# Performance work log

Hardware: AMD Instinct MI355X
Metric: run time of the kernel (lower is better)

Reference implementation:

```python
import jax, jax.numpy as jnp
import numpy as np

N_NODES = 100000
N_EDGES = 1600000
N_GRAPHS = 4096
IN_DIM = 14
HID = 128


def setup_inputs() -> dict:
    key = jax.random.key(0)
    ks = jax.random.split(key, 12)
    x = jax.random.normal(ks[0], (N_NODES, IN_DIM), dtype=jnp.float32)
    edge_index = jax.random.randint(ks[1], (2, N_EDGES), 0, N_NODES, dtype=jnp.int64)
    batch = jnp.sort(jax.random.randint(ks[2], (N_NODES,), 0, N_GRAPHS, dtype=jnp.int64))

    def lin(k, fan_in, fan_out):
        bound = 1.0 / np.sqrt(fan_in)
        kw, kb = jax.random.split(k)
        W = jax.random.uniform(kw, (fan_in, fan_out), minval=-bound, maxval=bound, dtype=jnp.float32)
        b = jax.random.uniform(kb, (fan_out,), minval=-bound, maxval=bound, dtype=jnp.float32)
        return W, b

    W1a, b1a = lin(ks[3], IN_DIM, HID)
    W1b, b1b = lin(ks[4], HID, HID)
    W2a, b2a = lin(ks[5], HID, HID)
    W2b, b2b = lin(ks[6], HID, HID)
    Wout, bout = lin(ks[7], HID, HID)
    return dict(x=x, edge_index=edge_index, batch=batch,
                W1a=W1a, b1a=b1a, W1b=W1b, b1b=b1b,
                W2a=W2a, b2a=b2a, W2b=W2b, b2b=b2b,
                Wout=Wout, bout=bout)


def _gin_conv(x, src, dst, Wa, ba, Wb, bb):
    # aggregate: sum of neighbor features x[src] scattered to dst; eps = 0
    agg = jax.ops.segment_sum(x[src], dst, num_segments=N_NODES)
    h = x + agg  # (1 + eps) * x + sum_j x_j, eps=0
    h = jax.nn.relu(h @ Wa + ba)
    return h @ Wb + bb


def reference(x, edge_index, batch, W1a, b1a, W1b, b1b, W2a, b2a, W2b, b2b, Wout, bout):
    src, dst = edge_index[0], edge_index[1]
    h = jax.nn.relu(_gin_conv(x, src, dst, W1a, b1a, W1b, b1b))
    h = jax.nn.relu(_gin_conv(h, src, dst, W2a, b2a, W2b, b2b))
    # global mean pool over graphs
    sums = jax.ops.segment_sum(h, batch, num_segments=N_GRAPHS)          # [G, HID]
    cnts = jax.ops.segment_sum(jnp.ones((h.shape[0],), h.dtype), batch, num_segments=N_GRAPHS)
    pooled = sums / jnp.maximum(cnts, 1.0)[:, None]
    # dropout is identity in eval mode
    return pooled @ Wout + bout
```

## Files before the change

kernel.cpp:

```cpp
#include <hip/hip_runtime.h>
#include <hip/hip_bf16.h>

#define NODES  100000
#define EDGES  1600000
#define GRAPHS 4096
#define HID    128
#define INDIM  14
#define NPART  8
#define PART_SZ ((NODES + NPART - 1) / NPART)
#define BPG    256
#define CSTRIDE 64
#define LDST   136

typedef float f32x4 __attribute__((ext_vector_type(4)));
typedef short bf16x8 __attribute__((ext_vector_type(8)));
typedef int   i32x4 __attribute__((ext_vector_type(4)));

__device__ __forceinline__ unsigned packbf(float a, float b) {
    __hip_bfloat162 t;
    t.x = __float2bfloat16(a);
    t.y = __float2bfloat16(b);
    return *(unsigned*)&t;
}
__device__ __forceinline__ void acc8(float* a, uint4 v) {
    a[0] += __uint_as_float(v.x << 16);
    a[1] += __uint_as_float(v.x & 0xffff0000u);
    a[2] += __uint_as_float(v.y << 16);
    a[3] += __uint_as_float(v.y & 0xffff0000u);
    a[4] += __uint_as_float(v.z << 16);
    a[5] += __uint_as_float(v.z & 0xffff0000u);
    a[6] += __uint_as_float(v.w << 16);
    a[7] += __uint_as_float(v.w & 0xffff0000u);
}


__global__ void k_zero_int(int* __restrict__ p, int n) {
    int i = blockIdx.x * 256 + threadIdx.x;
    if (i < n) p[i] = 0;
}

__global__ __launch_bounds__(256) void k_fill_fx(const i32x4* __restrict__ src4,
                                                 const i32x4* __restrict__ dst4,
                                                 int* __restrict__ cnt,
                                                 int* __restrict__ csr) {
    const int g = blockIdx.x & (NPART - 1);
    const int blk = blockIdx.x >> 3;
    const int lo = g * PART_SZ;
    const int n4 = EDGES / 4;
    for (int e4 = blk * 256 + threadIdx.x; e4 < n4; e4 += BPG * 256) {
        i32x4 d = __builtin_nontemporal_load(&dst4[e4]);
        i32x4 s = __builtin_nontemporal_load(&src4[e4]);
#pragma unroll
        for (int j = 0; j < 4; j++) {
            int dj = d[j];
            if ((unsigned)(dj - lo) < PART_SZ) {
                int pos = atomicAdd(&cnt[dj], 1);
                if (pos < CSTRIDE) csr[dj * CSTRIDE + pos] = s[j];
            }
        }
    }
}


__global__ void k_w_cvt4(const float* __restrict__ Wa, const float* __restrict__ Wb,
                         const float* __restrict__ Wc, const float* __restrict__ Wd,
                         __hip_bfloat16* __restrict__ Ta, __hip_bfloat16* __restrict__ Tb,
                         __hip_bfloat16* __restrict__ Tc, __hip_bfloat16* __restrict__ Td) {
    int which = blockIdx.x >> 6;
    int idx = (blockIdx.x & 63) * 256 + threadIdx.x;
    const float* W = which == 0 ? Wa : which == 1 ? Wb : which == 2 ? Wc : Wd;
    __hip_bfloat16* T = which == 0 ? Ta : which == 1 ? Tb : which == 2 ? Tc : Td;
    int n = idx & 127, k = idx >> 7;
    T[n * HID + k] = __float2bfloat16(W[k * HID + n]);
}

template <int RELU, int TO_LDS>
__device__ __forceinline__ void mfma_slice16(const __hip_bfloat16* lds_in,
                                             const __hip_bfloat16* __restrict__ Wt,
                                             const float* __restrict__ bias,
                                             __hip_bfloat16* lds_out,
                                             __hip_bfloat16* __restrict__ gout,
                                             int row0, int tid) {
    const int wave = tid >> 6;
    const int lane = tid & 63;
    const int rl = lane & 15;
    const int kb = lane >> 4;

    bf16x8 afrag[4];
#pragma unroll
    for (int kc = 0; kc < 4; kc++)
        afrag[kc] = *(const bf16x8*)(lds_in + rl * LDST + kc * 32 + kb * 8);

#pragma unroll
    for (int s = 0; s < 2; s++) {
        const int n = wave * 2 + s;
        f32x4 acc = (f32x4){0.f, 0.f, 0.f, 0.f};
        const __hip_bfloat16* Bp = Wt + (size_t)(n * 16 + rl) * HID + kb * 8;
#pragma unroll
        for (int kc = 0; kc < 4; kc++) {
            bf16x8 bfrag = *(const bf16x8*)(Bp + kc * 32);
            acc = __builtin_amdgcn_mfma_f32_16x16x32_bf16(afrag[kc], bfrag, acc, 0, 0, 0);
        }
        const int col = n * 16 + rl;
        const float bv = bias[col];
#pragma unroll
        for (int j = 0; j < 4; j++) {
            int rloc = kb * 4 + j;
            float v = acc[j] + bv;
            if (RELU) v = fmaxf(v, 0.f);
            if (TO_LDS)
                lds_out[rloc * LDST + col] = __float2bfloat16(v);
            else
                gout[(size_t)(row0 + rloc) * HID + col] = __float2bfloat16(v);
        }
    }
}


__global__ __launch_bounds__(256) void k_l1(const float* __restrict__ x,
                                            const int* __restrict__ cnt,
                                            const int* __restrict__ csr,
                                            const float* __restrict__ W1a,
                                            const float* __restrict__ b1a,
                                            const __hip_bfloat16* __restrict__ Wt1b,
                                            const float* __restrict__ b1b,
                                            __hip_bfloat16* __restrict__ h1) {
    __shared__ float p14[16][16];
    __shared__ __hip_bfloat16 t[16 * LDST];
    const int row0 = blockIdx.x * 16;
    const int tid = threadIdx.x;

    {
        int n = tid >> 4, d = tid & 15;
        int node = row0 + n;
        if (d < INDIM) {
            int len = cnt[node];
            if (len > CSTRIDE) len = CSTRIDE;
            const int* cp = csr + (size_t)node * CSTRIDE;
            float acc = x[node * INDIM + d];
            int e = 0;
            for (; e + 7 < len; e += 8) {
                int s0 = cp[e], s1 = cp[e + 1], s2 = cp[e + 2], s3 = cp[e + 3];
                int s4 = cp[e + 4], s5 = cp[e + 5], s6 = cp[e + 6], s7 = cp[e + 7];
                float v0 = x[s0 * INDIM + d], v1 = x[s1 * INDIM + d];
                float v2 = x[s2 * INDIM + d], v3 = x[s3 * INDIM + d];
                float v4 = x[s4 * INDIM + d], v5 = x[s5 * INDIM + d];
                float v6 = x[s6 * INDIM + d], v7 = x[s7 * INDIM + d];
                acc += ((v0 + v1) + (v2 + v3)) + ((v4 + v5) + (v6 + v7));
            }
            for (; e + 3 < len; e += 4) {
                int s0 = cp[e], s1 = cp[e + 1], s2 = cp[e + 2], s3 = cp[e + 3];
                acc += x[s0 * INDIM + d] + x[s1 * INDIM + d] +
                       x[s2 * INDIM + d] + x[s3 * INDIM + d];
            }
            for (; e < len; e++) acc += x[cp[e] * INDIM + d];
            p14[n][d] = acc;
        }
    }
    __syncthreads();

    for (int i = tid; i < 512; i += 256) {
        int r = i >> 5, c4 = (i & 31) << 2;
        float4 bv = *(const float4*)&b1a[c4];
        float ax = bv.x, ay = bv.y, az = bv.z, aw = bv.w;
#pragma unroll
        for (int k = 0; k < INDIM; k++) {
            float a = p14[r][k];
            float4 w = *(const float4*)&W1a[k * HID + c4];
            ax += a * w.x; ay += a * w.y; az += a * w.z; aw += a * w.w;
        }
        unsigned p0 = packbf(fmaxf(ax, 0.f), fmaxf(ay, 0.f));
        unsigned p1 = packbf(fmaxf(az, 0.f), fmaxf(aw, 0.f));
        *(uint2*)&t[r * LDST + c4] = make_uint2(p0, p1);
    }
    __syncthreads();

    mfma_slice16<1, 0>(t, Wt1b, b1b, nullptr, h1, row0, tid);
}


__global__ __launch_bounds__(256) void k_l2(const uint4* __restrict__ H,
                                            const int* __restrict__ cnt,
                                            const int* __restrict__ csr,
                                            const __hip_bfloat16* __restrict__ Wt2a,
                                            const float* __restrict__ b2a,
                                            const __hip_bfloat16* __restrict__ Wt2b,
                                            const float* __restrict__ b2b,
                                            __hip_bfloat16* __restrict__ h2) {
    __shared__ __hip_bfloat16 ta[16 * LDST];
    __shared__ __hip_bfloat16 tb[16 * LDST];
    const int row0 = blockIdx.x * 16;
    const int tid = threadIdx.x;

    {
        int n = tid >> 4, q = tid & 15;
        int node = row0 + n;
        int len = cnt[node];
        if (len > CSTRIDE) len = CSTRIDE;
        const int* cp = csr + (size_t)node * CSTRIDE;
        float a[8];
        uint4 v = H[(size_t)node * 16 + q];
        a[0] = __uint_as_float(v.x << 16);
        a[1] = __uint_as_float(v.x & 0xffff0000u);
        a[2] = __uint_as_float(v.y << 16);
        a[3] = __uint_as_float(v.y & 0xffff0000u);
        a[4] = __uint_as_float(v.z << 16);
        a[5] = __uint_as_float(v.z & 0xffff0000u);
        a[6] = __uint_as_float(v.w << 16);
        a[7] = __uint_as_float(v.w & 0xffff0000u);
        int e = 0;
        for (; e + 7 < len; e += 8) {
            uint4 v0 = H[(size_t)cp[e + 0] * 16 + q];
            uint4 v1 = H[(size_t)cp[e + 1] * 16 + q];
            uint4 v2 = H[(size_t)cp[e + 2] * 16 + q];
            uint4 v3 = H[(size_t)cp[e + 3] * 16 + q];
            uint4 v4 = H[(size_t)cp[e + 4] * 16 + q];
            uint4 v5 = H[(size_t)cp[e + 5] * 16 + q];
            uint4 v6 = H[(size_t)cp[e + 6] * 16 + q];
            uint4 v7 = H[(size_t)cp[e + 7] * 16 + q];
            acc8(a, v0); acc8(a, v1); acc8(a, v2); acc8(a, v3);
            acc8(a, v4); acc8(a, v5); acc8(a, v6); acc8(a, v7);
        }
        for (; e + 3 < len; e += 4) {
            uint4 v0 = H[(size_t)cp[e + 0] * 16 + q];
            uint4 v1 = H[(size_t)cp[e + 1] * 16 + q];
            uint4 v2 = H[(size_t)cp[e + 2] * 16 + q];
            uint4 v3 = H[(size_t)cp[e + 3] * 16 + q];
            acc8(a, v0); acc8(a, v1); acc8(a, v2); acc8(a, v3);
        }
        for (; e < len; e++) {
            uint4 vv = H[(size_t)cp[e] * 16 + q];
            acc8(a, vv);
        }
        uint4 o;
        o.x = packbf(a[0], a[1]);
        o.y = packbf(a[2], a[3]);
        o.z = packbf(a[4], a[5]);
        o.w = packbf(a[6], a[7]);
        *(uint4*)&ta[n * LDST + q * 8] = o;
    }
    __syncthreads();

    mfma_slice16<1, 1>(ta, Wt2a, b2a, tb, nullptr, row0, tid);
    __syncthreads();

    mfma_slice16<1, 0>(tb, Wt2b, b2b, nullptr, h2, row0, tid);
}


__global__ __launch_bounds__(256) void k_head(const __hip_bfloat16* __restrict__ A,
                                              const __hip_bfloat16* __restrict__ Wt,
                                              const float* __restrict__ bias,
                                              float* __restrict__ out) {
    const int wave = threadIdx.x >> 6;
    const int lane = threadIdx.x & 63;
    const int row0 = blockIdx.x * 64 + wave * 16;
    const int rl = lane & 15;
    const int kb = lane >> 4;

    const __hip_bfloat16* Ap = A + (size_t)(row0 + rl) * HID + kb * 8;
    bf16x8 afrag[4];
#pragma unroll
    for (int kc = 0; kc < 4; kc++) afrag[kc] = *(const bf16x8*)(Ap + kc * 32);

#pragma unroll
    for (int n = 0; n < 8; n++) {
        f32x4 acc = (f32x4){0.f, 0.f, 0.f, 0.f};
        const __hip_bfloat16* Bp = Wt + (size_t)(n * 16 + rl) * HID + kb * 8;
#pragma unroll
        for (int kc = 0; kc < 4; kc++) {
            bf16x8 bfrag = *(const bf16x8*)(Bp + kc * 32);
            acc = __builtin_amdgcn_mfma_f32_16x16x32_bf16(afrag[kc], bfrag, acc, 0, 0, 0);
        }
        const int col = n * 16 + rl;
        const float bv = bias[col];
#pragma unroll
        for (int j = 0; j < 4; j++)
            out[(size_t)(row0 + kb * 4 + j) * HID + col] = acc[j] + bv;
    }
}


__device__ __forceinline__ int lower_bound_i(const int* __restrict__ a, int n, int key) {
    int lo = 0, hi = n;
    while (lo < hi) {
        int mid = (lo + hi) >> 1;
        if (a[mid] < key) lo = mid + 1; else hi = mid;
    }
    return lo;
}

__global__ __launch_bounds__(128) void k_pool(const __hip_bfloat16* __restrict__ H,
                                              const int* __restrict__ batch,
                                              __hip_bfloat16* __restrict__ pooled) {
    int g = blockIdx.x;
    int d = threadIdx.x;
    int lo = lower_bound_i(batch, NODES, g);
    int hi = lower_bound_i(batch, NODES, g + 1);
    float acc = 0.f;
    for (int i = lo; i < hi; i++) acc += __bfloat162float(H[(size_t)i * HID + d]);
    float cnt = (float)(hi - lo);
    pooled[(size_t)g * HID + d] = __float2bfloat16(acc / fmaxf(cnt, 1.0f));
}


extern "C" void kernel_launch(void* const* d_in, const int* in_sizes, int n_in,
                              void* d_out, int out_size, void* d_ws, size_t ws_size,
                              hipStream_t stream) {
    const float* x     = (const float*)d_in[0];
    const int*   ei    = (const int*)d_in[1];
    const int*   batch = (const int*)d_in[2];
    const float* W1a = (const float*)d_in[3];
    const float* b1a = (const float*)d_in[4];
    const float* W1b = (const float*)d_in[5];
    const float* b1b = (const float*)d_in[6];
    const float* W2a = (const float*)d_in[7];
    const float* b2a = (const float*)d_in[8];
    const float* W2b = (const float*)d_in[9];
    const float* b2b = (const float*)d_in[10];
    const float* Wout = (const float*)d_in[11];
    const float* bout = (const float*)d_in[12];

    const int* src = ei;
    const int* dst = ei + EDGES;

    char* w = (char*)d_ws;
    auto alloc = [&](size_t bytes) {
        void* p = (void*)w;
        w += (bytes + 255) & ~(size_t)255;
        return p;
    };
    __hip_bfloat16* h1 = (__hip_bfloat16*)alloc((size_t)NODES * HID * 2);
    __hip_bfloat16* h2 = (__hip_bfloat16*)alloc((size_t)NODES * HID * 2);
    __hip_bfloat16* pooled = (__hip_bfloat16*)alloc((size_t)GRAPHS * HID * 2);
    __hip_bfloat16* Wt1b = (__hip_bfloat16*)alloc(HID * HID * 2);
    __hip_bfloat16* Wt2a = (__hip_bfloat16*)alloc(HID * HID * 2);
    __hip_bfloat16* Wt2b = (__hip_bfloat16*)alloc(HID * HID * 2);
    __hip_bfloat16* Wtout = (__hip_bfloat16*)alloc(HID * HID * 2);
    int* cnt = (int*)alloc((size_t)NODES * 4);
    int* csr = (int*)alloc((size_t)NODES * CSTRIDE * 4);
    float* out = (float*)d_out;

    k_w_cvt4<<<256, 256, 0, stream>>>(W1b, W2a, W2b, Wout, Wt1b, Wt2a, Wt2b, Wtout);

    k_zero_int<<<(NODES + 255) / 256, 256, 0, stream>>>(cnt, NODES);
    k_fill_fx<<<NPART * BPG, 256, 0, stream>>>((const i32x4*)src, (const i32x4*)dst, cnt, csr);

    k_l1<<<NODES / 16, 256, 0, stream>>>(x, cnt, csr, W1a, b1a, Wt1b, b1b, h1);
    k_l2<<<NODES / 16, 256, 0, stream>>>((const uint4*)h1, cnt, csr, Wt2a, b2a, Wt2b, b2b, h2);

    k_pool<<<GRAPHS, 128, 0, stream>>>(h2, batch, pooled);
    k_head<<<GRAPHS / 64, 256, 0, stream>>>(pooled, Wtout, bout, out);
}
```

Baseline: 274.1 us.

## Slice hidden features into 16-column planes for cache-local layer-2 gather

Layer 1 now writes h1 in a sliced layout of eight planes of 16 bf16 columns each. A new gather kernel aggregates neighbours one slice at a time, so each slice's working set (about 3.2MB) can stay cache-resident during the random gathers. The aggregation is split from the two layer-2 GEMMs, which move to a separate MFMA kernel over 64-row tiles. The input x is also pre-converted to padded bf16, and the weight-conversion and counter-zeroing launches are merged into one prep kernel. In exchange the aggregate is written to and read back from global memory, one extra launch is added, and x is rounded to bf16 before aggregation.

```diff
diff --git a/kernel.cpp b/kernel.cpp
--- a/kernel.cpp
+++ b/kernel.cpp
@@ -11,6 +11,7 @@
 #define BPG    256
 #define CSTRIDE 64
 #define LDST   136
+#define NSLICE 8
 
 typedef float f32x4 __attribute__((ext_vector_type(4)));
 typedef short bf16x8 __attribute__((ext_vector_type(8)));
@@ -22,22 +23,38 @@
     t.y = __float2bfloat16(b);
     return *(unsigned*)&t;
 }
-__device__ __forceinline__ void acc8(float* a, uint4 v) {
-    a[0] += __uint_as_float(v.x << 16);
-    a[1] += __uint_as_float(v.x & 0xffff0000u);
-    a[2] += __uint_as_float(v.y << 16);
-    a[3] += __uint_as_float(v.y & 0xffff0000u);
-    a[4] += __uint_as_float(v.z << 16);
-    a[5] += __uint_as_float(v.z & 0xffff0000u);
-    a[6] += __uint_as_float(v.w << 16);
-    a[7] += __uint_as_float(v.w & 0xffff0000u);
-}
-
-
-__global__ void k_zero_int(int* __restrict__ p, int n) {
-    int i = blockIdx.x * 256 + threadIdx.x;
-    if (i < n) p[i] = 0;
-}
+__device__ __forceinline__ float2 upk(unsigned u) {
+    float2 f;
+    f.x = __uint_as_float(u << 16);
+    f.y = __uint_as_float(u & 0xffff0000u);
+    return f;
+}
+
+
+__global__ void k_prep(const float* __restrict__ W1b, const float* __restrict__ W2a,
+                       const float* __restrict__ W2b, const float* __restrict__ Wout,
+                       __hip_bfloat16* __restrict__ T1b, __hip_bfloat16* __restrict__ T2a,
+                       __hip_bfloat16* __restrict__ T2b, __hip_bfloat16* __restrict__ Tout,
+                       const float* __restrict__ x, __hip_bfloat16* __restrict__ xb,
+                       int* __restrict__ cnt) {
+    int b = blockIdx.x;
+    if (b < 256) {
+        int which = b >> 6;
+        int idx = (b & 63) * 256 + threadIdx.x;
+        const float* W = which == 0 ? W1b : which == 1 ? W2a : which == 2 ? W2b : Wout;
+        __hip_bfloat16* T = which == 0 ? T1b : which == 1 ? T2a : which == 2 ? T2b : Tout;
+        int n = idx & 127, k = idx >> 7;
+        T[n * HID + k] = __float2bfloat16(W[k * HID + n]);
+    } else if (b < 256 + 6250) {
+        int idx = (b - 256) * 256 + threadIdx.x;
+        int node = idx >> 4, c = idx & 15;
+        xb[idx] = __float2bfloat16(c < INDIM ? x[node * INDIM + c] : 0.f);
+    } else {
+        int i = (b - 6506) * 256 + threadIdx.x;
+        if (i < NODES) cnt[i] = 0;
+    }
+}
+
 
 __global__ __launch_bounds__(256) void k_fill_fx(const i32x4* __restrict__ src4,
                                                  const i32x4* __restrict__ dst4,
@@ -62,69 +79,14 @@
 }
 
 
-__global__ void k_w_cvt4(const float* __restrict__ Wa, const float* __restrict__ Wb,
-                         const float* __restrict__ Wc, const float* __restrict__ Wd,
-                         __hip_bfloat16* __restrict__ Ta, __hip_bfloat16* __restrict__ Tb,
-                         __hip_bfloat16* __restrict__ Tc, __hip_bfloat16* __restrict__ Td) {
-    int which = blockIdx.x >> 6;
-    int idx = (blockIdx.x & 63) * 256 + threadIdx.x;
-    const float* W = which == 0 ? Wa : which == 1 ? Wb : which == 2 ? Wc : Wd;
-    __hip_bfloat16* T = which == 0 ? Ta : which == 1 ? Tb : which == 2 ? Tc : Td;
-    int n = idx & 127, k = idx >> 7;
-    T[n * HID + k] = __float2bfloat16(W[k * HID + n]);
-}
-
-template <int RELU, int TO_LDS>
-__device__ __forceinline__ void mfma_slice16(const __hip_bfloat16* lds_in,
-                                             const __hip_bfloat16* __restrict__ Wt,
-                                             const float* __restrict__ bias,
-                                             __hip_bfloat16* lds_out,
-                                             __hip_bfloat16* __restrict__ gout,
-                                             int row0, int tid) {
-    const int wave = tid >> 6;
-    const int lane = tid & 63;
-    const int rl = lane & 15;
-    const int kb = lane >> 4;
-
-    bf16x8 afrag[4];
-#pragma unroll
-    for (int kc = 0; kc < 4; kc++)
-        afrag[kc] = *(const bf16x8*)(lds_in + rl * LDST + kc * 32 + kb * 8);
-
-#pragma unroll
-    for (int s = 0; s < 2; s++) {
-        const int n = wave * 2 + s;
-        f32x4 acc = (f32x4){0.f, 0.f, 0.f, 0.f};
-        const __hip_bfloat16* Bp = Wt + (size_t)(n * 16 + rl) * HID + kb * 8;
-#pragma unroll
-        for (int kc = 0; kc < 4; kc++) {
-            bf16x8 bfrag = *(const bf16x8*)(Bp + kc * 32);
-            acc = __builtin_amdgcn_mfma_f32_16x16x32_bf16(afrag[kc], bfrag, acc, 0, 0, 0);
-        }
-        const int col = n * 16 + rl;
-        const float bv = bias[col];
-#pragma unroll
-        for (int j = 0; j < 4; j++) {
-            int rloc = kb * 4 + j;
-            float v = acc[j] + bv;
-            if (RELU) v = fmaxf(v, 0.f);
-            if (TO_LDS)
-                lds_out[rloc * LDST + col] = __float2bfloat16(v);
-            else
-                gout[(size_t)(row0 + rloc) * HID + col] = __float2bfloat16(v);
-        }
-    }
-}
-
-
-__global__ __launch_bounds__(256) void k_l1(const float* __restrict__ x,
+__global__ __launch_bounds__(256) void k_l1(const __hip_bfloat16* __restrict__ xb,
                                             const int* __restrict__ cnt,
                                             const int* __restrict__ csr,
                                             const float* __restrict__ W1a,
                                             const float* __restrict__ b1a,
                                             const __hip_bfloat16* __restrict__ Wt1b,
                                             const float* __restrict__ b1b,
-                                            __hip_bfloat16* __restrict__ h1) {
+                                            __hip_bfloat16* __restrict__ h1b) {
     __shared__ float p14[16][16];
     __shared__ __hip_bfloat16 t[16 * LDST];
     const int row0 = blockIdx.x * 16;
@@ -137,23 +99,17 @@
             int len = cnt[node];
             if (len > CSTRIDE) len = CSTRIDE;
             const int* cp = csr + (size_t)node * CSTRIDE;
-            float acc = x[node * INDIM + d];
+            float acc = __bfloat162float(xb[node * 16 + d]);
             int e = 0;
-            for (; e + 7 < len; e += 8) {
-                int s0 = cp[e], s1 = cp[e + 1], s2 = cp[e + 2], s3 = cp[e + 3];
-                int s4 = cp[e + 4], s5 = cp[e + 5], s6 = cp[e + 6], s7 = cp[e + 7];
-                float v0 = x[s0 * INDIM + d], v1 = x[s1 * INDIM + d];
-                float v2 = x[s2 * INDIM + d], v3 = x[s3 * INDIM + d];
-                float v4 = x[s4 * INDIM + d], v5 = x[s5 * INDIM + d];
-                float v6 = x[s6 * INDIM + d], v7 = x[s7 * INDIM + d];
-                acc += ((v0 + v1) + (v2 + v3)) + ((v4 + v5) + (v6 + v7));
-            }
             for (; e + 3 < len; e += 4) {
                 int s0 = cp[e], s1 = cp[e + 1], s2 = cp[e + 2], s3 = cp[e + 3];
-                acc += x[s0 * INDIM + d] + x[s1 * INDIM + d] +
-                       x[s2 * INDIM + d] + x[s3 * INDIM + d];
+                float v0 = __bfloat162float(xb[s0 * 16 + d]);
+                float v1 = __bfloat162float(xb[s1 * 16 + d]);
+                float v2 = __bfloat162float(xb[s2 * 16 + d]);
+                float v3 = __bfloat162float(xb[s3 * 16 + d]);
+                acc += (v0 + v1) + (v2 + v3);
             }
-            for (; e < len; e++) acc += x[cp[e] * INDIM + d];
+            for (; e < len; e++) acc += __bfloat162float(xb[cp[e] * 16 + d]);
             p14[n][d] = acc;
         }
     }
@@ -175,108 +131,144 @@
     }
     __syncthreads();
 
-    mfma_slice16<1, 0>(t, Wt1b, b1b, nullptr, h1, row0, tid);
-}
-
-
-__global__ __launch_bounds__(256) void k_l2(const uint4* __restrict__ H,
-                                            const int* __restrict__ cnt,
-                                            const int* __restrict__ csr,
+    {
+        const int wave = tid >> 6;
+        const int lane = tid & 63;
+        const int rl = lane & 15;
+        const int kb = lane >> 4;
+        bf16x8 afrag[4];
+#pragma unroll
+        for (int kc = 0; kc < 4; kc++)
+            afrag[kc] = *(const bf16x8*)(t + rl * LDST + kc * 32 + kb * 8);
+#pragma unroll
+        for (int s = 0; s < 2; s++) {
+            const int n = wave * 2 + s;
+            f32x4 acc = (f32x4){0.f, 0.f, 0.f, 0.f};
+            const __hip_bfloat16* Bp = Wt1b + (size_t)(n * 16 + rl) * HID + kb * 8;
+#pragma unroll
+            for (int kc = 0; kc < 4; kc++) {
+                bf16x8 bfrag = *(const bf16x8*)(Bp + kc * 32);
+                acc = __builtin_amdgcn_mfma_f32_16x16x32_bf16(afrag[kc], bfrag, acc, 0, 0, 0);
+            }
+            const float bv = b1b[n * 16 + rl];
+#pragma unroll
+            for (int j = 0; j < 4; j++) {
+                int node = row0 + kb * 4 + j;
+                float v = fmaxf(acc[j] + bv, 0.f);
+                h1b[((size_t)n * NODES + node) * 16 + rl] = __float2bfloat16(v);
+            }
+        }
+    }
+}
+
+
+__global__ __launch_bounds__(256) void k_g(const unsigned* __restrict__ Hb,
+                                           const int* __restrict__ cnt,
+                                           const int* __restrict__ csr,
+                                           unsigned* __restrict__ Ab) {
+    const int s = blockIdx.x & 7;
+    const int tile = blockIdx.x >> 3;
+    const int nl = threadIdx.x >> 3;
+    const int q = threadIdx.x & 7;
+    const int node = tile * 32 + nl;
+    const unsigned* base = Hb + (size_t)s * NODES * 8;
+    int len = cnt[node];
+    if (len > CSTRIDE) len = CSTRIDE;
+    const int* cp = csr + (size_t)node * CSTRIDE;
+    float2 acc = upk(base[(size_t)node * 8 + q]);
+    int e = 0;
+    for (; e + 7 < len; e += 8) {
+        unsigned v0 = base[(size_t)cp[e + 0] * 8 + q];
+        unsigned v1 = base[(size_t)cp[e + 1] * 8 + q];
+        unsigned v2 = base[(size_t)cp[e + 2] * 8 + q];
+        unsigned v3 = base[(size_t)cp[e + 3] * 8 + q];
+        unsigned v4 = base[(size_t)cp[e + 4] * 8 + q];
+        unsigned v5 = base[(size_t)cp[e + 5] * 8 + q];
+        unsigned v6 = base[(size_t)cp[e + 6] * 8 + q];
+        unsigned v7 = base[(size_t)cp[e + 7] * 8 + q];
+        float2 f0 = upk(v0), f1 = upk(v1), f2 = upk(v2), f3 = upk(v3);
+        float2 f4 = upk(v4), f5 = upk(v5), f6 = upk(v6), f7 = upk(v7);
+        acc.x += ((f0.x + f1.x) + (f2.x + f3.x)) + ((f4.x + f5.x) + (f6.x + f7.x));
+        acc.y += ((f0.y + f1.y) + (f2.y + f3.y)) + ((f4.y + f5.y) + (f6.y + f7.y));
+    }
+    for (; e + 3 < len; e += 4) {
+        unsigned v0 = base[(size_t)cp[e + 0] * 8 + q];
+        unsigned v1 = base[(size_t)cp[e + 1] * 8 + q];
+        unsigned v2 = base[(size_t)cp[e + 2] * 8 + q];
+        unsigned v3 = base[(size_t)cp[e + 3] * 8 + q];
+        float2 f0 = upk(v0), f1 = upk(v1), f2 = upk(v2), f3 = upk(v3);
+        acc.x += (f0.x + f1.x) + (f2.x + f3.x);
+        acc.y += (f0.y + f1.y) + (f2.y + f3.y);
+    }
+    for (; e < len; e++) {
+        float2 f = upk(base[(size_t)cp[e] * 8 + q]);
+        acc.x += f.x;
+        acc.y += f.y;
+    }
+    Ab[(size_t)s * NODES * 8 + (size_t)node * 8 + q] = packbf(acc.x, acc.y);
+}
+
+
+__global__ __launch_bounds__(256) void k_g2(const __hip_bfloat16* __restrict__ aggb,
                                             const __hip_bfloat16* __restrict__ Wt2a,
                                             const float* __restrict__ b2a,
                                             const __hip_bfloat16* __restrict__ Wt2b,
                                             const float* __restrict__ b2b,
                                             __hip_bfloat16* __restrict__ h2) {
-    __shared__ __hip_bfloat16 ta[16 * LDST];
-    __shared__ __hip_bfloat16 tb[16 * LDST];
-    const int row0 = blockIdx.x * 16;
-    const int tid = threadIdx.x;
-
-    {
-        int n = tid >> 4, q = tid & 15;
-        int node = row0 + n;
-        int len = cnt[node];
-        if (len > CSTRIDE) len = CSTRIDE;
-        const int* cp = csr + (size_t)node * CSTRIDE;
-        float a[8];
-        uint4 v = H[(size_t)node * 16 + q];
-        a[0] = __uint_as_float(v.x << 16);
-        a[1] = __uint_as_float(v.x & 0xffff0000u);
-        a[2] = __uint_as_float(v.y << 16);
-        a[3] = __uint_as_float(v.y & 0xffff0000u);
-        a[4] = __uint_as_float(v.z << 16);
-        a[5] = __uint_as_float(v.z & 0xffff0000u);
-        a[6] = __uint_as_float(v.w << 16);
-        a[7] = __uint_as_float(v.w & 0xffff0000u);
-        int e = 0;
-        for (; e + 7 < len; e += 8) {
-            uint4 v0 = H[(size_t)cp[e + 0] * 16 + q];
-            uint4 v1 = H[(size_t)cp[e + 1] * 16 + q];
-            uint4 v2 = H[(size_t)cp[e + 2] * 16 + q];
-            uint4 v3 = H[(size_t)cp[e + 3] * 16 + q];
-            uint4 v4 = H[(size_t)cp[e + 4] * 16 + q];
-            uint4 v5 = H[(size_t)cp[e + 5] * 16 + q];
-            uint4 v6 = H[(size_t)cp[e + 6] * 16 + q];
-            uint4 v7 = H[(size_t)cp[e + 7] * 16 + q];
-            acc8(a, v0); acc8(a, v1); acc8(a, v2); acc8(a, v3);
-            acc8(a, v4); acc8(a, v5); acc8(a, v6); acc8(a, v7);
-        }
-        for (; e + 3 < len; e += 4) {
-            uint4 v0 = H[(size_t)cp[e + 0] * 16 + q];
-            uint4 v1 = H[(size_t)cp[e + 1] * 16 + q];
-            uint4 v2 = H[(size_t)cp[e + 2] * 16 + q];
-            uint4 v3 = H[(size_t)cp[e + 3] * 16 + q];
-            acc8(a, v0); acc8(a, v1); acc8(a, v2); acc8(a, v3);
-        }
-        for (; e < len; e++) {
-            uint4 vv = H[(size_t)cp[e] * 16 + q];
-            acc8(a, vv);
-        }
-        uint4 o;
-        o.x = packbf(a[0], a[1]);
-        o.y = packbf(a[2], a[3]);
-        o.z = packbf(a[4], a[5]);
-        o.w = packbf(a[6], a[7]);
-        *(uint4*)&ta[n * LDST + q * 8] = o;
-    }
-    __syncthreads();
-
-    mfma_slice16<1, 1>(ta, Wt2a, b2a, tb, nullptr, row0, tid);
-    __syncthreads();
-
-    mfma_slice16<1, 0>(tb, Wt2b, b2b, nullptr, h2, row0, tid);
-}
-
-
-__global__ __launch_bounds__(256) void k_head(const __hip_bfloat16* __restrict__ A,
-                                              const __hip_bfloat16* __restrict__ Wt,
-                                              const float* __restrict__ bias,
-                                              float* __restrict__ out) {
+    __shared__ __hip_bfloat16 t[64 * LDST];
     const int wave = threadIdx.x >> 6;
     const int lane = threadIdx.x & 63;
-    const int row0 = blockIdx.x * 64 + wave * 16;
     const int rl = lane & 15;
     const int kb = lane >> 4;
-
-    const __hip_bfloat16* Ap = A + (size_t)(row0 + rl) * HID + kb * 8;
+    const int row0 = blockIdx.x * 64;
+
+    int arow = row0 + wave * 16 + rl;
+    if (arow > NODES - 1) arow = NODES - 1;
+
     bf16x8 afrag[4];
 #pragma unroll
-    for (int kc = 0; kc < 4; kc++) afrag[kc] = *(const bf16x8*)(Ap + kc * 32);
+    for (int kc = 0; kc < 4; kc++) {
+        int slice = kc * 2 + (kb >> 1);
+        afrag[kc] = *(const bf16x8*)(aggb + ((size_t)slice * NODES + arow) * 16 + (kb & 1) * 8);
+    }
 
 #pragma unroll
     for (int n = 0; n < 8; n++) {
         f32x4 acc = (f32x4){0.f, 0.f, 0.f, 0.f};
-        const __hip_bfloat16* Bp = Wt + (size_t)(n * 16 + rl) * HID + kb * 8;
+        const __hip_bfloat16* Bp = Wt2a + (size_t)(n * 16 + rl) * HID + kb * 8;
 #pragma unroll
         for (int kc = 0; kc < 4; kc++) {
             bf16x8 bfrag = *(const bf16x8*)(Bp + kc * 32);
             acc = __builtin_amdgcn_mfma_f32_16x16x32_bf16(afrag[kc], bfrag, acc, 0, 0, 0);
         }
         const int col = n * 16 + rl;
-        const float bv = bias[col];
+        const float bv = b2a[col];
 #pragma unroll
         for (int j = 0; j < 4; j++)
-            out[(size_t)(row0 + kb * 4 + j) * HID + col] = acc[j] + bv;
+            t[(wave * 16 + kb * 4 + j) * LDST + col] = __float2bfloat16(fmaxf(acc[j] + bv, 0.f));
+    }
+    __syncthreads();
+
+#pragma unroll
+    for (int kc = 0; kc < 4; kc++)
+        afrag[kc] = *(const bf16x8*)(t + (wave * 16 + rl) * LDST + kc * 32 + kb * 8);
+#pragma unroll
+    for (int n = 0; n < 8; n++) {
+        f32x4 acc = (f32x4){0.f, 0.f, 0.f, 0.f};
+        const __hip_bfloat16* Bp = Wt2b + (size_t)(n * 16 + rl) * HID + kb * 8;
+#pragma unroll
+        for (int kc = 0; kc < 4; kc++) {
+            bf16x8 bfrag = *(const bf16x8*)(Bp + kc * 32);
+            acc = __builtin_amdgcn_mfma_f32_16x16x32_bf16(afrag[kc], bfrag, acc, 0, 0, 0);
+        }
+        const int col = n * 16 + rl;
+        const float bv = b2b[col];
+#pragma unroll
+        for (int j = 0; j < 4; j++) {
+            int row = row0 + wave * 16 + kb * 4 + j;
+            if (row < NODES)
+                h2[(size_t)row * HID + col] = __float2bfloat16(fmaxf(acc[j] + bv, 0.f));
+        }
     }
 }
 
@@ -301,6 +293,39 @@
     for (int i = lo; i < hi; i++) acc += __bfloat162float(H[(size_t)i * HID + d]);
     float cnt = (float)(hi - lo);
     pooled[(size_t)g * HID + d] = __float2bfloat16(acc / fmaxf(cnt, 1.0f));
+}
+
+
+__global__ __launch_bounds__(256) void k_head(const __hip_bfloat16* __restrict__ A,
+                                              const __hip_bfloat16* __restrict__ Wt,
+                                              const float* __restrict__ bias,
+                                              float* __restrict__ out) {
+    const int wave = threadIdx.x >> 6;
+    const int lane = threadIdx.x & 63;
+    const int row0 = blockIdx.x * 64 + wave * 16;
+    const int rl = lane & 15;
+    const int kb = lane >> 4;
+
+    const __hip_bfloat16* Ap = A + (size_t)(row0 + rl) * HID + kb * 8;
+    bf16x8 afrag[4];
+#pragma unroll
+    for (int kc = 0; kc < 4; kc++) afrag[kc] = *(const bf16x8*)(Ap + kc * 32);
+
+#pragma unroll
+    for (int n = 0; n < 8; n++) {
+        f32x4 acc = (f32x4){0.f, 0.f, 0.f, 0.f};
+        const __hip_bfloat16* Bp = Wt + (size_t)(n * 16 + rl) * HID + kb * 8;
+#pragma unroll
+        for (int kc = 0; kc < 4; kc++) {
+            bf16x8 bfrag = *(const bf16x8*)(Bp + kc * 32);
+            acc = __builtin_amdgcn_mfma_f32_16x16x32_bf16(afrag[kc], bfrag, acc, 0, 0, 0);
+        }
+        const int col = n * 16 + rl;
+        const float bv = bias[col];
+#pragma unroll
+        for (int j = 0; j < 4; j++)
+            out[(size_t)(row0 + kb * 4 + j) * HID + col] = acc[j] + bv;
+    }
 }
 
 
@@ -330,8 +355,10 @@
         w += (bytes + 255) & ~(size_t)255;
         return p;
     };
-    __hip_bfloat16* h1 = (__hip_bfloat16*)alloc((size_t)NODES * HID * 2);
-    __hip_bfloat16* h2 = (__hip_bfloat16*)alloc((size_t)NODES * HID * 2);
+    __hip_bfloat16* xb   = (__hip_bfloat16*)alloc((size_t)NODES * 16 * 2);
+    __hip_bfloat16* h1b  = (__hip_bfloat16*)alloc((size_t)NSLICE * NODES * 16 * 2);
+    __hip_bfloat16* aggb = (__hip_bfloat16*)alloc((size_t)NSLICE * NODES * 16 * 2);
+    __hip_bfloat16* h2   = (__hip_bfloat16*)alloc((size_t)NODES * HID * 2);
     __hip_bfloat16* pooled = (__hip_bfloat16*)alloc((size_t)GRAPHS * HID * 2);
     __hip_bfloat16* Wt1b = (__hip_bfloat16*)alloc(HID * HID * 2);
     __hip_bfloat16* Wt2a = (__hip_bfloat16*)alloc(HID * HID * 2);
@@ -341,13 +368,15 @@
     int* csr = (int*)alloc((size_t)NODES * CSTRIDE * 4);
     float* out = (float*)d_out;
 
-    k_w_cvt4<<<256, 256, 0, stream>>>(W1b, W2a, W2b, Wout, Wt1b, Wt2a, Wt2b, Wtout);
-
-    k_zero_int<<<(NODES + 255) / 256, 256, 0, stream>>>(cnt, NODES);
+    k_prep<<<6897, 256, 0, stream>>>(W1b, W2a, W2b, Wout, Wt1b, Wt2a, Wt2b, Wtout, x, xb, cnt);
+
     k_fill_fx<<<NPART * BPG, 256, 0, stream>>>((const i32x4*)src, (const i32x4*)dst, cnt, csr);
 
-    k_l1<<<NODES / 16, 256, 0, stream>>>(x, cnt, csr, W1a, b1a, Wt1b, b1b, h1);
-    k_l2<<<NODES / 16, 256, 0, stream>>>((const uint4*)h1, cnt, csr, Wt2a, b2a, Wt2b, b2b, h2);
+    k_l1<<<NODES / 16, 256, 0, stream>>>(xb, cnt, csr, W1a, b1a, Wt1b, b1b, h1b);
+
+    k_g<<<(NODES / 32) * NSLICE, 256, 0, stream>>>((const unsigned*)h1b, cnt, csr,
+                                                   (unsigned*)aggb);
+    k_g2<<<(NODES + 63) / 64, 256, 0, stream>>>(aggb, Wt2a, b2a, Wt2b, b2b, h2);
 
     k_pool<<<GRAPHS, 128, 0, stream>>>(h2, batch, pooled);
     k_head<<<GRAPHS / 64, 256, 0, stream>>>(pooled, Wtout, bout, out);
```

New measurement: 325.4 us. +18.7%, slower.

## Fuse global mean pooling into layer-2 kernel via segmented atomic sums

Applied to the files above, without the earlier changes.

The second GIN layer kernel now keeps its ReLU output in fp32 shared memory and reduces each 16-row tile by graph id, atomically adding partial sums into an fp32 pooled buffer. This removes the h2 round trip to global memory and the separate pooling kernel, which ran a serial per-graph loop. The head kernel now computes graph node counts by binary search and applies the mean scaling itself. The cost is float atomics with nondeterministic ordering, plus a larger zero-init kernel.

```diff
diff --git a/kernel.cpp b/kernel.cpp
--- a/kernel.cpp
+++ b/kernel.cpp
@@ -11,6 +11,7 @@
 #define BPG    256
 #define CSTRIDE 64
 #define LDST   136
+#define LDSTF  132
 
 typedef float f32x4 __attribute__((ext_vector_type(4)));
 typedef short bf16x8 __attribute__((ext_vector_type(8)));
@@ -34,10 +35,12 @@
 }
 
 
-__global__ void k_zero_int(int* __restrict__ p, int n) {
+__global__ void k_zero2(int* __restrict__ cnt, float* __restrict__ pooled) {
     int i = blockIdx.x * 256 + threadIdx.x;
-    if (i < n) p[i] = 0;
-}
+    if (i < NODES) cnt[i] = 0;
+    if (i < GRAPHS * HID) pooled[i] = 0.f;
+}
+
 
 __global__ __launch_bounds__(256) void k_fill_fx(const i32x4* __restrict__ src4,
                                                  const i32x4* __restrict__ dst4,
@@ -73,6 +76,7 @@
     int n = idx & 127, k = idx >> 7;
     T[n * HID + k] = __float2bfloat16(W[k * HID + n]);
 }
+
 
 template <int RELU, int TO_LDS>
 __device__ __forceinline__ void mfma_slice16(const __hip_bfloat16* lds_in,
@@ -179,18 +183,23 @@
 }
 
 
-__global__ __launch_bounds__(256) void k_l2(const uint4* __restrict__ H,
-                                            const int* __restrict__ cnt,
-                                            const int* __restrict__ csr,
-                                            const __hip_bfloat16* __restrict__ Wt2a,
-                                            const float* __restrict__ b2a,
-                                            const __hip_bfloat16* __restrict__ Wt2b,
-                                            const float* __restrict__ b2b,
-                                            __hip_bfloat16* __restrict__ h2) {
+__global__ __launch_bounds__(256) void k_l2p(const uint4* __restrict__ H,
+                                             const int* __restrict__ cnt,
+                                             const int* __restrict__ csr,
+                                             const int* __restrict__ batch,
+                                             const __hip_bfloat16* __restrict__ Wt2a,
+                                             const float* __restrict__ b2a,
+                                             const __hip_bfloat16* __restrict__ Wt2b,
+                                             const float* __restrict__ b2b,
+                                             float* __restrict__ pooled) {
     __shared__ __hip_bfloat16 ta[16 * LDST];
     __shared__ __hip_bfloat16 tb[16 * LDST];
+    __shared__ float t2f[16 * LDSTF];
+    __shared__ int sb[16];
     const int row0 = blockIdx.x * 16;
     const int tid = threadIdx.x;
+
+    if (tid < 16) sb[tid] = batch[row0 + tid];
 
     {
         int n = tid >> 4, q = tid & 15;
@@ -244,11 +253,66 @@
     mfma_slice16<1, 1>(ta, Wt2a, b2a, tb, nullptr, row0, tid);
     __syncthreads();
 
-    mfma_slice16<1, 0>(tb, Wt2b, b2b, nullptr, h2, row0, tid);
-}
-
-
-__global__ __launch_bounds__(256) void k_head(const __hip_bfloat16* __restrict__ A,
+    {
+        const int wave = tid >> 6;
+        const int lane = tid & 63;
+        const int rl = lane & 15;
+        const int kb = lane >> 4;
+        bf16x8 afrag[4];
+#pragma unroll
+        for (int kc = 0; kc < 4; kc++)
+            afrag[kc] = *(const bf16x8*)(tb + rl * LDST + kc * 32 + kb * 8);
+#pragma unroll
+        for (int s = 0; s < 2; s++) {
+            const int n = wave * 2 + s;
+            f32x4 acc = (f32x4){0.f, 0.f, 0.f, 0.f};
+            const __hip_bfloat16* Bp = Wt2b + (size_t)(n * 16 + rl) * HID + kb * 8;
+#pragma unroll
+            for (int kc = 0; kc < 4; kc++) {
+                bf16x8 bfrag = *(const bf16x8*)(Bp + kc * 32);
+                acc = __builtin_amdgcn_mfma_f32_16x16x32_bf16(afrag[kc], bfrag, acc, 0, 0, 0);
+            }
+            const int col = n * 16 + rl;
+            const float bv = b2b[col];
+#pragma unroll
+            for (int j = 0; j < 4; j++)
+                t2f[(kb * 4 + j) * LDSTF + col] = fmaxf(acc[j] + bv, 0.f);
+        }
+    }
+    __syncthreads();
+
+    {
+        int c = tid & 127;
+        int half = tid >> 7;
+        int r0 = half * 8;
+        float acc = t2f[r0 * LDSTF + c];
+        int gprev = sb[r0];
+        for (int r = r0 + 1; r < r0 + 8; r++) {
+            int g = sb[r];
+            float v = t2f[r * LDSTF + c];
+            if (g != gprev) {
+                atomicAdd(&pooled[(size_t)gprev * HID + c], acc);
+                acc = 0.f;
+                gprev = g;
+            }
+            acc += v;
+        }
+        atomicAdd(&pooled[(size_t)gprev * HID + c], acc);
+    }
+}
+
+
+__device__ __forceinline__ int lower_bound_i(const int* __restrict__ a, int n, int key) {
+    int lo = 0, hi = n;
+    while (lo < hi) {
+        int mid = (lo + hi) >> 1;
+        if (a[mid] < key) lo = mid + 1; else hi = mid;
+    }
+    return lo;
+}
+
+__global__ __launch_bounds__(256) void k_head(const float* __restrict__ pooled,
+                                              const int* __restrict__ batch,
                                               const __hip_bfloat16* __restrict__ Wt,
                                               const float* __restrict__ bias,
                                               float* __restrict__ out) {
@@ -258,10 +322,20 @@
     const int rl = lane & 15;
     const int kb = lane >> 4;
 
-    const __hip_bfloat16* Ap = A + (size_t)(row0 + rl) * HID + kb * 8;
+    const int g = row0 + rl;
+    int lo = lower_bound_i(batch, NODES, g);
+    int hi = lower_bound_i(batch, NODES, g + 1);
+    float inv = 1.0f / fmaxf((float)(hi - lo), 1.0f);
+
     bf16x8 afrag[4];
 #pragma unroll
-    for (int kc = 0; kc < 4; kc++) afrag[kc] = *(const bf16x8*)(Ap + kc * 32);
+    for (int kc = 0; kc < 4; kc++) {
+        const float* Ap = pooled + (size_t)g * HID + kc * 32 + kb * 8;
+        unsigned u[4];
+#pragma unroll
+        for (int p = 0; p < 4; p++) u[p] = packbf(Ap[p * 2] * inv, Ap[p * 2 + 1] * inv);
+        afrag[kc] = *(bf16x8*)u;
+    }
 
 #pragma unroll
     for (int n = 0; n < 8; n++) {
@@ -278,29 +352,6 @@
         for (int j = 0; j < 4; j++)
             out[(size_t)(row0 + kb * 4 + j) * HID + col] = acc[j] + bv;
     }
-}
-
-
-__device__ __forceinline__ int lower_bound_i(const int* __restrict__ a, int n, int key) {
-    int lo = 0, hi = n;
-    while (lo < hi) {
-        int mid = (lo + hi) >> 1;
-        if (a[mid] < key) lo = mid + 1; else hi = mid;
-    }
-    return lo;
-}
-
-__global__ __launch_bounds__(128) void k_pool(const __hip_bfloat16* __restrict__ H,
-                                              const int* __restrict__ batch,
-                                              __hip_bfloat16* __restrict__ pooled) {
-    int g = blockIdx.x;
-    int d = threadIdx.x;
-    int lo = lower_bound_i(batch, NODES, g);
-    int hi = lower_bound_i(batch, NODES, g + 1);
-    float acc = 0.f;
-    for (int i = lo; i < hi; i++) acc += __bfloat162float(H[(size_t)i * HID + d]);
-    float cnt = (float)(hi - lo);
-    pooled[(size_t)g * HID + d] = __float2bfloat16(acc / fmaxf(cnt, 1.0f));
 }
 
 
@@ -331,24 +382,24 @@
         return p;
     };
     __hip_bfloat16* h1 = (__hip_bfloat16*)alloc((size_t)NODES * HID * 2);
-    __hip_bfloat16* h2 = (__hip_bfloat16*)alloc((size_t)NODES * HID * 2);
-    __hip_bfloat16* pooled = (__hip_bfloat16*)alloc((size_t)GRAPHS * HID * 2);
+    int* cnt = (int*)alloc((size_t)NODES * 4);
+    float* pooled = (float*)alloc((size_t)GRAPHS * HID * 4);
     __hip_bfloat16* Wt1b = (__hip_bfloat16*)alloc(HID * HID * 2);
     __hip_bfloat16* Wt2a = (__hip_bfloat16*)alloc(HID * HID * 2);
     __hip_bfloat16* Wt2b = (__hip_bfloat16*)alloc(HID * HID * 2);
     __hip_bfloat16* Wtout = (__hip_bfloat16*)alloc(HID * HID * 2);
-    int* cnt = (int*)alloc((size_t)NODES * 4);
     int* csr = (int*)alloc((size_t)NODES * CSTRIDE * 4);
     float* out = (float*)d_out;
 
     k_w_cvt4<<<256, 256, 0, stream>>>(W1b, W2a, W2b, Wout, Wt1b, Wt2a, Wt2b, Wtout);
-
-    k_zero_int<<<(NODES + 255) / 256, 256, 0, stream>>>(cnt, NODES);
+    k_zero2<<<(GRAPHS * HID + 255) / 256, 256, 0, stream>>>(cnt, pooled);
+
     k_fill_fx<<<NPART * BPG, 256, 0, stream>>>((const i32x4*)src, (const i32x4*)dst, cnt, csr);
 
     k_l1<<<NODES / 16, 256, 0, stream>>>(x, cnt, csr, W1a, b1a, Wt1b, b1b, h1);
-    k_l2<<<NODES / 16, 256, 0, stream>>>((const uint4*)h1, cnt, csr, Wt2a, b2a, Wt2b, b2b, h2);
-
-    k_pool<<<GRAPHS, 128, 0, stream>>>(h2, batch, pooled);
-    k_head<<<GRAPHS / 64, 256, 0, stream>>>(pooled, Wtout, bout, out);
-}
+
+    k_l2p<<<NODES / 16, 256, 0, stream>>>((const uint4*)h1, cnt, csr, batch,
+                                          Wt2a, b2a, Wt2b, b2b, pooled);
+
+    k_head<<<GRAPHS / 64, 256, 0, stream>>>(pooled, batch, Wtout, bout, out);
+}
```

New measurement: 257.4 us. -6.1%, faster.
